# Kernel tuning notes

Hardware: AMD Instinct MI355X
Metric: run time of the kernel (lower is better)

## Reference

```python
import jax, jax.numpy as jnp
import numpy as np

OUT_SIZE = 7      # roi_layer out_size
SAMPLE_NUM = 2    # roi_layer sample_num
STRIDES = (4, 8, 16, 32)
IMG = 1024.0


def _roi_align(feat_nchw, rois, out, scale, sn):
    """mmdet RoIAlign (aligned=False), vectorized over all rois.

    feat_nchw: [B, C, H, W]; rois: [N, 5] = (batch_idx, x1, y1, x2, y2).
    Returns [N, C, out, out].
    """
    feat = jnp.transpose(feat_nchw, (0, 2, 3, 1))  # [B, H, W, C]
    B, H, W, C = feat.shape
    N = rois.shape[0]
    b = rois[:, 0].astype(jnp.int32)
    x1 = rois[:, 1] * scale
    y1 = rois[:, 2] * scale
    x2 = rois[:, 3] * scale
    y2 = rois[:, 4] * scale
    roi_w = jnp.maximum(x2 - x1, 1.0)
    roi_h = jnp.maximum(y2 - y1, 1.0)
    # sample-point offsets within the roi, in bin units: [out*sn]
    grid = (jnp.arange(out, dtype=jnp.float32)[:, None]
            + (jnp.arange(sn, dtype=jnp.float32)[None, :] + 0.5) / sn).reshape(-1)
    ys = y1[:, None] + grid[None, :] * (roi_h / out)[:, None]  # [N, S]
    xs = x1[:, None] + grid[None, :] * (roi_w / out)[:, None]  # [N, S]

    def interp1(coord, size):
        valid = ((coord > -1.0) & (coord < size)).astype(coord.dtype)
        c = jnp.clip(coord, 0.0, size - 1.0)
        lo = jnp.floor(c).astype(jnp.int32)
        hi = jnp.minimum(lo + 1, size - 1)
        w_hi = c - lo.astype(coord.dtype)
        w_lo = 1.0 - w_hi
        # zero-out out-of-image samples via the weights
        return lo, hi, w_lo * valid, w_hi * valid

    y_lo, y_hi, wy_lo, wy_hi = interp1(ys, H)
    x_lo, x_hi, wx_lo, wx_hi = interp1(xs, W)

    def gather(yi, xi):
        # [N, S, S, C]
        return feat[b[:, None, None], yi[:, :, None], xi[:, None, :]]

    val = (gather(y_lo, x_lo) * (wy_lo[:, :, None] * wx_lo[:, None, :])[..., None]
           + gather(y_lo, x_hi) * (wy_lo[:, :, None] * wx_hi[:, None, :])[..., None]
           + gather(y_hi, x_lo) * (wy_hi[:, :, None] * wx_lo[:, None, :])[..., None]
           + gather(y_hi, x_hi) * (wy_hi[:, :, None] * wx_hi[:, None, :])[..., None])
    # average the sn x sn samples inside each bin
    val = val.reshape(N, out, sn, out, sn, C).mean(axis=(2, 4))  # [N, out, out, C]
    return jnp.transpose(val, (0, 3, 1, 2))  # [N, C, out, out]


def setup_inputs() -> dict:
    key = jax.random.key(0)
    ks = jax.random.split(key, 8)
    feats = {}
    for i, hw in enumerate([256, 128, 64, 32]):
        feats[f"feat{i}"] = jax.random.normal(ks[i], (1, 256, hw, hw), dtype=jnp.float32)
    N = 1000
    u = jax.random.uniform(ks[4], (N, 4), dtype=jnp.float32)
    x1 = u[:, 0] * (IMG - 64.0)
    y1 = u[:, 1] * (IMG - 64.0)
    w = 16.0 + u[:, 2] * 480.0
    h = 16.0 + u[:, 3] * 480.0
    x2 = jnp.minimum(x1 + w, IMG - 1.0)
    y2 = jnp.minimum(y1 + h, IMG - 1.0)
    bidx = jnp.zeros((N,), dtype=jnp.float32)
    rois = jnp.stack([bidx, x1, y1, x2, y2], axis=1)
    feats["rois"] = rois
    return feats


def reference(feat0, feat1, feat2, feat3, rois):
    feats = (feat0, feat1, feat2, feat3)
    # PASingleRoIExtractor multi-level path: RoIAlign every roi on every level,
    # then elementwise max across levels.
    out = _roi_align(feats[0], rois, OUT_SIZE, 1.0 / STRIDES[0], SAMPLE_NUM)
    for lvl in range(1, len(feats)):
        out = jnp.maximum(out, _roi_align(feats[lvl], rois, OUT_SIZE,
                                          1.0 / STRIDES[lvl], SAMPLE_NUM))
    return out
```

## Files before the change

kernel.cpp:

```cpp
#include <hip/hip_runtime.h>


#define NCH 256
#define NBIN 49

__device__ __constant__ int   d_H[4]      = {256, 128, 64, 32};
__device__ __constant__ float d_scale[4]  = {0.25f, 0.125f, 0.0625f, 0.03125f};
__device__ __constant__ int   d_off4[4]   = {0, 2097152, 2621440, 2752512};
__device__ __constant__ size_t d_offu[4]  = {0, 16777216, 20971520, 22020096};
__device__ __constant__ int   d_tstart[4] = {0, 4096, 5120, 5376};
__device__ __constant__ int   d_tilesx[4] = {4, 2, 1, 1};

__device__ __forceinline__ unsigned rne_bf16(float v) {
    unsigned b = __float_as_uint(v);
    b += 0x7fffu + ((b >> 16) & 1u);
    return b >> 16;
}

__device__ __forceinline__ int4 make_entry(float coord, int size, int mult) {
    float valid = (coord > -1.0f && coord < (float)size) ? 1.0f : 0.0f;
    float c = fminf(fmaxf(coord, 0.0f), (float)size - 1.0f);
    int lo = (int)floorf(c);
    int hi = min(lo + 1, size - 1);
    float whi = (c - (float)lo) * valid;
    float wlo = (1.0f - (c - (float)lo)) * valid;
    int4 r;
    r.x = lo * mult;
    r.y = hi * mult;
    r.z = __float_as_int(wlo);
    r.w = __float_as_int(whi);
    return r;
}

__device__ __forceinline__ void acc8(float* acc, uint4 u, float w) {
    acc[0] = fmaf(w, __uint_as_float(u.x << 16),         acc[0]);
    acc[1] = fmaf(w, __uint_as_float(u.x & 0xffff0000u), acc[1]);
    acc[2] = fmaf(w, __uint_as_float(u.y << 16),         acc[2]);
    acc[3] = fmaf(w, __uint_as_float(u.y & 0xffff0000u), acc[3]);
    acc[4] = fmaf(w, __uint_as_float(u.z << 16),         acc[4]);
    acc[5] = fmaf(w, __uint_as_float(u.z & 0xffff0000u), acc[5]);
    acc[6] = fmaf(w, __uint_as_float(u.w << 16),         acc[6]);
    acc[7] = fmaf(w, __uint_as_float(u.w & 0xffff0000u), acc[7]);
}

__device__ __forceinline__ void do_sample(const uint4* __restrict__ base,
                                          float* acc, int4 ye, int4 xe) {
    float wyl = __int_as_float(ye.z), wyh = __int_as_float(ye.w);
    float wxl = __int_as_float(xe.z), wxh = __int_as_float(xe.w);
    uint4 ull = base[ye.x + xe.x];
    uint4 ulh = base[ye.x + xe.y];
    uint4 uhl = base[ye.y + xe.x];
    uint4 uhh = base[ye.y + xe.y];
    acc8(acc, ull, wyl * wxl);
    acc8(acc, ulh, wyl * wxh);
    acc8(acc, uhl, wyh * wxl);
    acc8(acc, uhh, wyh * wxh);
}

__global__ __launch_bounds__(256) void transpose_fused(
    const float* __restrict__ f0, const float* __restrict__ f1,
    const float* __restrict__ f2, const float* __restrict__ f3,
    unsigned short* __restrict__ out) {
    __shared__ float tile[64][65];

    const int bid = blockIdx.x;
    const int lvl = (bid >= d_tstart[1]) + (bid >= d_tstart[2]) + (bid >= d_tstart[3]);
    int rem = bid - d_tstart[lvl];
    const int H = d_H[lvl];
    const int tnx = d_tilesx[lvl];
    const int xt = rem % tnx; rem /= tnx;
    const int y  = rem % H;
    const int cg = rem / H;
    const int W = H;
    const int x0 = xt * 64;
    const float* in = (lvl == 0) ? f0 : (lvl == 1) ? f1 : (lvl == 2) ? f2 : f3;
    unsigned short* o = out + d_offu[lvl];

    const int tid = threadIdx.x;
    const int tx = tid & 63;
    const int tq = tid >> 6;
    const size_t HW = (size_t)H * W;
    const float* inp = in + (size_t)(cg * 64) * HW + (size_t)y * W + x0;
    const bool xin = (x0 + tx) < W;
#pragma unroll
    for (int r = 0; r < 16; ++r) {
        int cl = tq * 16 + r;
        tile[cl][tx] = xin ? inp[(size_t)cl * HW + tx] : 0.0f;
    }
    __syncthreads();

    const int o8 = tid & 7;
    const int xi = tid >> 3;
#pragma unroll
    for (int pass = 0; pass < 2; ++pass) {
        int px = xi + pass * 32;
        int x = x0 + px;
        if (x < W) {
            unsigned w0, w1, w2, w3;
            w0 = rne_bf16(tile[o8 * 8 + 0][px]) | (rne_bf16(tile[o8 * 8 + 1][px]) << 16);
            w1 = rne_bf16(tile[o8 * 8 + 2][px]) | (rne_bf16(tile[o8 * 8 + 3][px]) << 16);
            w2 = rne_bf16(tile[o8 * 8 + 4][px]) | (rne_bf16(tile[o8 * 8 + 5][px]) << 16);
            w3 = rne_bf16(tile[o8 * 8 + 6][px]) | (rne_bf16(tile[o8 * 8 + 7][px]) << 16);
            uint4* dst = (uint4*)(o + (size_t)(y * W + x) * NCH + cg * 64 + o8 * 8);
            *dst = make_uint4(w0, w1, w2, w3);
        }
    }
}

__global__ __launch_bounds__(256) void roi_main2(
    const uint4* __restrict__ ws, const float* __restrict__ rois,
    float* __restrict__ out) {
    __shared__ float4 smem4[128 * NBIN / 4];
    __shared__ int4 tbl[4][2][14];
    float* smem = (float*)smem4;

    const int n    = blockIdx.x >> 1;
    const int half = blockIdx.x & 1;
    const int tid  = threadIdx.x;
    const float* r = rois + (size_t)n * 5;

    if (tid < 112) {
        int lvl = tid / 28;
        int e = tid % 28;
        int axis = e / 14;
        int s = e % 14;
        int H = d_H[lvl];
        float sc = d_scale[lvl];
        float a  = (axis ? r[1] : r[2]) * sc;
        float b2 = (axis ? r[3] : r[4]) * sc;
        float binsz = fmaxf(b2 - a, 1.0f) * (1.0f / 7.0f);
        float g = (float)(s >> 1) + 0.25f + 0.5f * (float)(s & 1);
        float coord = a + g * binsz;
        int mult = axis ? 32 : H * 32;
        tbl[lvl][axis][s] = make_entry(coord, H, mult);
    }
    __syncthreads();

    const int p = tid & 15;
    const int h = tid >> 4;
    const int octet = half * 16 + p;
    const int bstart = (h * NBIN) >> 4;
    const int bend   = ((h + 1) * NBIN) >> 4;

    for (int b = bstart; b < bend; ++b) {
        int by = b / 7;
        int bx = b - by * 7;
        float m[8];
#pragma unroll
        for (int k = 0; k < 8; ++k) m[k] = -3.402823e38f;
#pragma unroll
        for (int lvl = 0; lvl < 4; ++lvl) {
            const uint4* base = ws + d_off4[lvl] + octet;
            int4 ye0 = tbl[lvl][0][2 * by];
            int4 ye1 = tbl[lvl][0][2 * by + 1];
            int4 xe0 = tbl[lvl][1][2 * bx];
            int4 xe1 = tbl[lvl][1][2 * bx + 1];
            float acc[8];
#pragma unroll
            for (int k = 0; k < 8; ++k) acc[k] = 0.0f;
            do_sample(base, acc, ye0, xe0);
            do_sample(base, acc, ye0, xe1);
            do_sample(base, acc, ye1, xe0);
            do_sample(base, acc, ye1, xe1);
#pragma unroll
            for (int k = 0; k < 8; ++k) m[k] = fmaxf(m[k], acc[k] * 0.25f);
        }
#pragma unroll
        for (int k = 0; k < 8; ++k) smem[(p * 8 + k) * NBIN + b] = m[k];
    }
    __syncthreads();

    float4* o4 = (float4*)(out + (size_t)n * (NCH * NBIN) + (size_t)half * (128 * NBIN));
    for (int i = tid; i < 128 * NBIN / 4; i += 256) o4[i] = smem4[i];
}

__global__ __launch_bounds__(256) void roi_direct(
    const float* __restrict__ f0, const float* __restrict__ f1,
    const float* __restrict__ f2, const float* __restrict__ f3,
    const float* __restrict__ rois, float* __restrict__ out) {
    const int n = blockIdx.x;
    const int c = threadIdx.x;
    const float* feats[4] = {f0, f1, f2, f3};
    const float* r = rois + (size_t)n * 5;
    for (int b = 0; b < NBIN; ++b) {
        int by = b / 7;
        int bx = b - by * 7;
        float m = -3.402823e38f;
#pragma unroll
        for (int lvl = 0; lvl < 4; ++lvl) {
            int H = d_H[lvl];
            float sc = d_scale[lvl];
            float x1 = r[1] * sc, y1 = r[2] * sc, x2 = r[3] * sc, y2 = r[4] * sc;
            float bw = fmaxf(x2 - x1, 1.0f) * (1.0f / 7.0f);
            float bh = fmaxf(y2 - y1, 1.0f) * (1.0f / 7.0f);
            const float* f = feats[lvl] + (size_t)c * H * H;
            float acc = 0.0f;
#pragma unroll
            for (int sy = 0; sy < 2; ++sy) {
#pragma unroll
                for (int sx = 0; sx < 2; ++sx) {
                    float yc = y1 + ((float)by + 0.25f + 0.5f * sy) * bh;
                    float xc = x1 + ((float)bx + 0.25f + 0.5f * sx) * bw;
                    int4 ey = make_entry(yc, H, H);
                    int4 ex = make_entry(xc, H, 1);
                    float wyl = __int_as_float(ey.z), wyh = __int_as_float(ey.w);
                    float wxl = __int_as_float(ex.z), wxh = __int_as_float(ex.w);
                    acc += f[ey.x + ex.x] * wyl * wxl + f[ey.x + ex.y] * wyl * wxh
                         + f[ey.y + ex.x] * wyh * wxl + f[ey.y + ex.y] * wyh * wxh;
                }
            }
            m = fmaxf(m, acc * 0.25f);
        }
        out[((size_t)n * NCH + c) * NBIN + b] = m;
    }
}

extern "C" void kernel_launch(void* const* d_in, const int* in_sizes, int n_in,
                              void* d_out, int out_size, void* d_ws, size_t ws_size,
                              hipStream_t stream) {
    const float* f0 = (const float*)d_in[0];
    const float* f1 = (const float*)d_in[1];
    const float* f2 = (const float*)d_in[2];
    const float* f3 = (const float*)d_in[3];
    const float* rois = (const float*)d_in[4];
    const int nrois = in_sizes[4] / 5;
    float* out = (float*)d_out;

    const size_t need = 44564480;
    if (ws_size >= need) {
        unsigned short* ws = (unsigned short*)d_ws;
        transpose_fused<<<5504, 256, 0, stream>>>(f0, f1, f2, f3, ws);
        roi_main2<<<2 * nrois, 256, 0, stream>>>((const uint4*)d_ws, rois, out);
    } else {
        roi_direct<<<nrois, 256, 0, stream>>>(f0, f1, f2, f3, rois, out);
    }
}
```

Measured before the change: 247.2 us.

## Switch workspace to fp16 with fdot2 accumulation and split each ROI into quarter-channel blocks

The channel-last workspace now holds fp16 instead of bf16, and the bilinear accumulation uses packed fp16 weights with the fdot2 instruction, so two taps are combined per instruction. The transpose loads use float2 with a padded tile. The ROI kernel now launches four blocks per ROI, each covering 64 channels, which doubles parallelism and shrinks shared memory per block. In exchange the fp16 weights and products carry reduced precision and overflow risk, and the per-ROI table setup is repeated across more blocks.

```diff
diff --git a/kernel.cpp b/kernel.cpp
--- a/kernel.cpp
+++ b/kernel.cpp
@@ -4,20 +4,209 @@
 #define NCH 256
 #define NBIN 49
 
-__device__ __constant__ int   d_H[4]      = {256, 128, 64, 32};
-__device__ __constant__ float d_scale[4]  = {0.25f, 0.125f, 0.0625f, 0.03125f};
-__device__ __constant__ int   d_off4[4]   = {0, 2097152, 2621440, 2752512};
-__device__ __constant__ size_t d_offu[4]  = {0, 16777216, 20971520, 22020096};
-__device__ __constant__ int   d_tstart[4] = {0, 4096, 5120, 5376};
-__device__ __constant__ int   d_tilesx[4] = {4, 2, 1, 1};
-
-__device__ __forceinline__ unsigned rne_bf16(float v) {
-    unsigned b = __float_as_uint(v);
-    b += 0x7fffu + ((b >> 16) & 1u);
-    return b >> 16;
-}
-
-__device__ __forceinline__ int4 make_entry(float coord, int size, int mult) {
+typedef _Float16 half2v __attribute__((ext_vector_type(2)));
+
+#if defined(__has_builtin)
+#if __has_builtin(__builtin_amdgcn_fdot2)
+#define HAVE_FDOT2 1
+#endif
+#if __has_builtin(__builtin_amdgcn_cvt_pkrtz)
+#define HAVE_PKRTZ 1
+#endif
+#endif
+
+__device__ __constant__ int    d_H[4]      = {256, 128, 64, 32};
+__device__ __constant__ float  d_scale[4]  = {0.25f, 0.125f, 0.0625f, 0.03125f};
+__device__ __constant__ int    d_off4[4]   = {0, 2097152, 2621440, 2752512};
+__device__ __constant__ size_t d_offu[4]   = {0, 16777216, 20971520, 22020096};
+__device__ __constant__ int    d_tstart[4] = {0, 4096, 5120, 5376};
+__device__ __constant__ int    d_tilesx[4] = {4, 2, 1, 1};
+
+__device__ __forceinline__ int pack_h2(float a, float b) {
+#ifdef HAVE_PKRTZ
+    return __builtin_bit_cast(int, __builtin_amdgcn_cvt_pkrtz(a, b));
+#else
+    half2v h;
+    h.x = (_Float16)a;
+    h.y = (_Float16)b;
+    return __builtin_bit_cast(int, h);
+#endif
+}
+__device__ __forceinline__ half2v bc_h2(int x) { return __builtin_bit_cast(half2v, x); }
+__device__ __forceinline__ half2v bc_h2u(unsigned x) { return __builtin_bit_cast(half2v, x); }
+
+#ifdef HAVE_FDOT2
+#define ACC2(uLLc, uLHc, w2, k0)                                                                       \
+    acc[k0] = __builtin_amdgcn_fdot2(bc_h2u(__builtin_amdgcn_perm((uLHc), (uLLc), 0x05040100u)), (w2), \
+                                     acc[k0], false);                                                  \
+    acc[k0 + 1] = __builtin_amdgcn_fdot2(                                                              \
+        bc_h2u(__builtin_amdgcn_perm((uLHc), (uLLc), 0x07060302u)), (w2), acc[k0 + 1], false)
+#else
+#define ACC2(uLLc, uLHc, w2, k0)                                       \
+    do {                                                               \
+        half2v a_ = bc_h2u(uLLc), b_ = bc_h2u(uLHc);                   \
+        float w0_ = (float)(w2).x, w1_ = (float)(w2).y;                \
+        acc[k0]     = fmaf((float)a_.x, w0_, acc[k0]);                 \
+        acc[k0]     = fmaf((float)b_.x, w1_, acc[k0]);                 \
+        acc[k0 + 1] = fmaf((float)a_.y, w0_, acc[k0 + 1]);             \
+        acc[k0 + 1] = fmaf((float)b_.y, w1_, acc[k0 + 1]);             \
+    } while (0)
+#endif
+
+__device__ __forceinline__ void do_sample(const uint4* __restrict__ base, float* acc, int4 ye,
+                                          int4 xe) {
+    uint4 uLL = base[ye.x + xe.x];
+    uint4 uLH = base[ye.x + xe.y];
+    uint4 uHL = base[ye.y + xe.x];
+    uint4 uHH = base[ye.y + xe.y];
+    half2v wx = bc_h2(xe.z);
+    half2v wlo = bc_h2(ye.z) * wx;
+    half2v whi = bc_h2(ye.w) * wx;
+    ACC2(uLL.x, uLH.x, wlo, 0);
+    ACC2(uLL.y, uLH.y, wlo, 2);
+    ACC2(uLL.z, uLH.z, wlo, 4);
+    ACC2(uLL.w, uLH.w, wlo, 6);
+    ACC2(uHL.x, uHH.x, whi, 0);
+    ACC2(uHL.y, uHH.y, whi, 2);
+    ACC2(uHL.z, uHH.z, whi, 4);
+    ACC2(uHL.w, uHH.w, whi, 6);
+}
+
+__global__ __launch_bounds__(256) void transpose_fused(
+    const float* __restrict__ f0, const float* __restrict__ f1, const float* __restrict__ f2,
+    const float* __restrict__ f3, unsigned short* __restrict__ out) {
+    __shared__ float tile[64 * 66];
+
+    const int bid = blockIdx.x;
+    const int lvl = (bid >= d_tstart[1]) + (bid >= d_tstart[2]) + (bid >= d_tstart[3]);
+    int rem = bid - d_tstart[lvl];
+    const int H = d_H[lvl];
+    const int tnx = d_tilesx[lvl];
+    const int xt = rem % tnx;
+    rem /= tnx;
+    const int y = rem % H;
+    const int cg = rem / H;
+    const int x0 = xt * 64;
+    const float* in = (lvl == 0) ? f0 : (lvl == 1) ? f1 : (lvl == 2) ? f2 : f3;
+    unsigned short* o = out + d_offu[lvl];
+
+    const int tid = threadIdx.x;
+    const int tx2 = tid & 31;
+    const int wv = tid >> 5;
+    const size_t HW = (size_t)H * H;
+    const float* inp = in + (size_t)(cg * 64) * HW + (size_t)y * H + x0;
+    const bool xin = (x0 + tx2 * 2) < H;
+#pragma unroll
+    for (int r = 0; r < 8; ++r) {
+        int cl = wv * 8 + r;
+        float2 v = make_float2(0.0f, 0.0f);
+        if (xin) v = *(const float2*)(inp + (size_t)cl * HW + tx2 * 2);
+        *(float2*)&tile[cl * 66 + tx2 * 2] = v;
+    }
+    __syncthreads();
+
+    const int o8 = tid & 7;
+    const int xi = tid >> 3;
+#pragma unroll
+    for (int pass = 0; pass < 2; ++pass) {
+        int px = xi + pass * 32;
+        int x = x0 + px;
+        if (x < H) {
+            const float* col = &tile[o8 * 8 * 66 + px];
+            unsigned d0 = (unsigned)pack_h2(col[0 * 66], col[1 * 66]);
+            unsigned d1 = (unsigned)pack_h2(col[2 * 66], col[3 * 66]);
+            unsigned d2 = (unsigned)pack_h2(col[4 * 66], col[5 * 66]);
+            unsigned d3 = (unsigned)pack_h2(col[6 * 66], col[7 * 66]);
+            uint4* dst = (uint4*)(o + (size_t)(y * H + x) * NCH + cg * 64 + o8 * 8);
+            *dst = make_uint4(d0, d1, d2, d3);
+        }
+    }
+}
+
+__global__ __launch_bounds__(256) void roi_main4(const uint4* __restrict__ ws,
+                                                 const float* __restrict__ rois,
+                                                 float* __restrict__ out) {
+    __shared__ float smem[64 * NBIN];
+    __shared__ int4 tbl[4][2][14];
+
+    const int n = blockIdx.x >> 2;
+    const int quarter = blockIdx.x & 3;
+    const int tid = threadIdx.x;
+    const float* r = rois + (size_t)n * 5;
+
+    if (tid < 112) {
+        int lvl = tid / 28;
+        int e = tid % 28;
+        int axis = e / 14;
+        int s = e % 14;
+        int H = d_H[lvl];
+        float sc = d_scale[lvl];
+        float a = (axis ? r[1] : r[2]) * sc;
+        float b2 = (axis ? r[3] : r[4]) * sc;
+        float binsz = fmaxf(b2 - a, 1.0f) * (1.0f / 7.0f);
+        float g = (float)(s >> 1) + 0.25f + 0.5f * (float)(s & 1);
+        float coord = a + g * binsz;
+        float valid = (coord > -1.0f && coord < (float)H) ? 1.0f : 0.0f;
+        float c = fminf(fmaxf(coord, 0.0f), (float)H - 1.0f);
+        int lo = (int)floorf(c);
+        int hi = min(lo + 1, H - 1);
+        float whi = (c - (float)lo) * valid;
+        float wlo = (1.0f - (c - (float)lo)) * valid;
+        int mult = axis ? 32 : H * 32;
+        int4 t;
+        t.x = lo * mult;
+        t.y = hi * mult;
+        if (axis) {
+            t.z = pack_h2(wlo, whi);
+            t.w = 0;
+        } else {
+            t.z = pack_h2(wlo, wlo);
+            t.w = pack_h2(whi, whi);
+        }
+        tbl[lvl][axis][s] = t;
+    }
+    __syncthreads();
+
+    const int p = tid & 7;
+    const int h = tid >> 3;
+    const int octet = quarter * 8 + p;
+    const int bstart = (h * NBIN) >> 5;
+    const int bend = ((h + 1) * NBIN) >> 5;
+
+    for (int b = bstart; b < bend; ++b) {
+        int by = b / 7;
+        int bx = b - by * 7;
+        float m[8];
+#pragma unroll
+        for (int k = 0; k < 8; ++k) m[k] = -3.402823e38f;
+#pragma unroll
+        for (int lvl = 0; lvl < 4; ++lvl) {
+            const uint4* base = ws + d_off4[lvl] + octet;
+            int4 ye0 = tbl[lvl][0][2 * by];
+            int4 ye1 = tbl[lvl][0][2 * by + 1];
+            int4 xe0 = tbl[lvl][1][2 * bx];
+            int4 xe1 = tbl[lvl][1][2 * bx + 1];
+            float acc[8];
+#pragma unroll
+            for (int k = 0; k < 8; ++k) acc[k] = 0.0f;
+            do_sample(base, acc, ye0, xe0);
+            do_sample(base, acc, ye0, xe1);
+            do_sample(base, acc, ye1, xe0);
+            do_sample(base, acc, ye1, xe1);
+#pragma unroll
+            for (int k = 0; k < 8; ++k) m[k] = fmaxf(m[k], acc[k] * 0.25f);
+        }
+#pragma unroll
+        for (int k = 0; k < 8; ++k) smem[(p * 8 + k) * NBIN + b] = m[k];
+    }
+    __syncthreads();
+
+    float4* o4 = (float4*)(out + (size_t)n * (NCH * NBIN) + (size_t)quarter * (64 * NBIN));
+    const float4* s4 = (const float4*)smem;
+    for (int i = tid; i < 64 * NBIN / 4; i += 256) o4[i] = s4[i];
+}
+
+__device__ __forceinline__ int4 make_entry_f(float coord, int size, int mult) {
     float valid = (coord > -1.0f && coord < (float)size) ? 1.0f : 0.0f;
     float c = fminf(fmaxf(coord, 0.0f), (float)size - 1.0f);
     int lo = (int)floorf(c);
@@ -32,152 +221,9 @@
     return r;
 }
 
-__device__ __forceinline__ void acc8(float* acc, uint4 u, float w) {
-    acc[0] = fmaf(w, __uint_as_float(u.x << 16),         acc[0]);
-    acc[1] = fmaf(w, __uint_as_float(u.x & 0xffff0000u), acc[1]);
-    acc[2] = fmaf(w, __uint_as_float(u.y << 16),         acc[2]);
-    acc[3] = fmaf(w, __uint_as_float(u.y & 0xffff0000u), acc[3]);
-    acc[4] = fmaf(w, __uint_as_float(u.z << 16),         acc[4]);
-    acc[5] = fmaf(w, __uint_as_float(u.z & 0xffff0000u), acc[5]);
-    acc[6] = fmaf(w, __uint_as_float(u.w << 16),         acc[6]);
-    acc[7] = fmaf(w, __uint_as_float(u.w & 0xffff0000u), acc[7]);
-}
-
-__device__ __forceinline__ void do_sample(const uint4* __restrict__ base,
-                                          float* acc, int4 ye, int4 xe) {
-    float wyl = __int_as_float(ye.z), wyh = __int_as_float(ye.w);
-    float wxl = __int_as_float(xe.z), wxh = __int_as_float(xe.w);
-    uint4 ull = base[ye.x + xe.x];
-    uint4 ulh = base[ye.x + xe.y];
-    uint4 uhl = base[ye.y + xe.x];
-    uint4 uhh = base[ye.y + xe.y];
-    acc8(acc, ull, wyl * wxl);
-    acc8(acc, ulh, wyl * wxh);
-    acc8(acc, uhl, wyh * wxl);
-    acc8(acc, uhh, wyh * wxh);
-}
-
-__global__ __launch_bounds__(256) void transpose_fused(
-    const float* __restrict__ f0, const float* __restrict__ f1,
-    const float* __restrict__ f2, const float* __restrict__ f3,
-    unsigned short* __restrict__ out) {
-    __shared__ float tile[64][65];
-
-    const int bid = blockIdx.x;
-    const int lvl = (bid >= d_tstart[1]) + (bid >= d_tstart[2]) + (bid >= d_tstart[3]);
-    int rem = bid - d_tstart[lvl];
-    const int H = d_H[lvl];
-    const int tnx = d_tilesx[lvl];
-    const int xt = rem % tnx; rem /= tnx;
-    const int y  = rem % H;
-    const int cg = rem / H;
-    const int W = H;
-    const int x0 = xt * 64;
-    const float* in = (lvl == 0) ? f0 : (lvl == 1) ? f1 : (lvl == 2) ? f2 : f3;
-    unsigned short* o = out + d_offu[lvl];
-
-    const int tid = threadIdx.x;
-    const int tx = tid & 63;
-    const int tq = tid >> 6;
-    const size_t HW = (size_t)H * W;
-    const float* inp = in + (size_t)(cg * 64) * HW + (size_t)y * W + x0;
-    const bool xin = (x0 + tx) < W;
-#pragma unroll
-    for (int r = 0; r < 16; ++r) {
-        int cl = tq * 16 + r;
-        tile[cl][tx] = xin ? inp[(size_t)cl * HW + tx] : 0.0f;
-    }
-    __syncthreads();
-
-    const int o8 = tid & 7;
-    const int xi = tid >> 3;
-#pragma unroll
-    for (int pass = 0; pass < 2; ++pass) {
-        int px = xi + pass * 32;
-        int x = x0 + px;
-        if (x < W) {
-            unsigned w0, w1, w2, w3;
-            w0 = rne_bf16(tile[o8 * 8 + 0][px]) | (rne_bf16(tile[o8 * 8 + 1][px]) << 16);
-            w1 = rne_bf16(tile[o8 * 8 + 2][px]) | (rne_bf16(tile[o8 * 8 + 3][px]) << 16);
-            w2 = rne_bf16(tile[o8 * 8 + 4][px]) | (rne_bf16(tile[o8 * 8 + 5][px]) << 16);
-            w3 = rne_bf16(tile[o8 * 8 + 6][px]) | (rne_bf16(tile[o8 * 8 + 7][px]) << 16);
-            uint4* dst = (uint4*)(o + (size_t)(y * W + x) * NCH + cg * 64 + o8 * 8);
-            *dst = make_uint4(w0, w1, w2, w3);
-        }
-    }
-}
-
-__global__ __launch_bounds__(256) void roi_main2(
-    const uint4* __restrict__ ws, const float* __restrict__ rois,
-    float* __restrict__ out) {
-    __shared__ float4 smem4[128 * NBIN / 4];
-    __shared__ int4 tbl[4][2][14];
-    float* smem = (float*)smem4;
-
-    const int n    = blockIdx.x >> 1;
-    const int half = blockIdx.x & 1;
-    const int tid  = threadIdx.x;
-    const float* r = rois + (size_t)n * 5;
-
-    if (tid < 112) {
-        int lvl = tid / 28;
-        int e = tid % 28;
-        int axis = e / 14;
-        int s = e % 14;
-        int H = d_H[lvl];
-        float sc = d_scale[lvl];
-        float a  = (axis ? r[1] : r[2]) * sc;
-        float b2 = (axis ? r[3] : r[4]) * sc;
-        float binsz = fmaxf(b2 - a, 1.0f) * (1.0f / 7.0f);
-        float g = (float)(s >> 1) + 0.25f + 0.5f * (float)(s & 1);
-        float coord = a + g * binsz;
-        int mult = axis ? 32 : H * 32;
-        tbl[lvl][axis][s] = make_entry(coord, H, mult);
-    }
-    __syncthreads();
-
-    const int p = tid & 15;
-    const int h = tid >> 4;
-    const int octet = half * 16 + p;
-    const int bstart = (h * NBIN) >> 4;
-    const int bend   = ((h + 1) * NBIN) >> 4;
-
-    for (int b = bstart; b < bend; ++b) {
-        int by = b / 7;
-        int bx = b - by * 7;
-        float m[8];
-#pragma unroll
-        for (int k = 0; k < 8; ++k) m[k] = -3.402823e38f;
-#pragma unroll
-        for (int lvl = 0; lvl < 4; ++lvl) {
-            const uint4* base = ws + d_off4[lvl] + octet;
-            int4 ye0 = tbl[lvl][0][2 * by];
-            int4 ye1 = tbl[lvl][0][2 * by + 1];
-            int4 xe0 = tbl[lvl][1][2 * bx];
-            int4 xe1 = tbl[lvl][1][2 * bx + 1];
-            float acc[8];
-#pragma unroll
-            for (int k = 0; k < 8; ++k) acc[k] = 0.0f;
-            do_sample(base, acc, ye0, xe0);
-            do_sample(base, acc, ye0, xe1);
-            do_sample(base, acc, ye1, xe0);
-            do_sample(base, acc, ye1, xe1);
-#pragma unroll
-            for (int k = 0; k < 8; ++k) m[k] = fmaxf(m[k], acc[k] * 0.25f);
-        }
-#pragma unroll
-        for (int k = 0; k < 8; ++k) smem[(p * 8 + k) * NBIN + b] = m[k];
-    }
-    __syncthreads();
-
-    float4* o4 = (float4*)(out + (size_t)n * (NCH * NBIN) + (size_t)half * (128 * NBIN));
-    for (int i = tid; i < 128 * NBIN / 4; i += 256) o4[i] = smem4[i];
-}
-
 __global__ __launch_bounds__(256) void roi_direct(
-    const float* __restrict__ f0, const float* __restrict__ f1,
-    const float* __restrict__ f2, const float* __restrict__ f3,
-    const float* __restrict__ rois, float* __restrict__ out) {
+    const float* __restrict__ f0, const float* __restrict__ f1, const float* __restrict__ f2,
+    const float* __restrict__ f3, const float* __restrict__ rois, float* __restrict__ out) {
     const int n = blockIdx.x;
     const int c = threadIdx.x;
     const float* feats[4] = {f0, f1, f2, f3};
@@ -201,12 +247,12 @@
                 for (int sx = 0; sx < 2; ++sx) {
                     float yc = y1 + ((float)by + 0.25f + 0.5f * sy) * bh;
                     float xc = x1 + ((float)bx + 0.25f + 0.5f * sx) * bw;
-                    int4 ey = make_entry(yc, H, H);
-                    int4 ex = make_entry(xc, H, 1);
+                    int4 ey = make_entry_f(yc, H, H);
+                    int4 ex = make_entry_f(xc, H, 1);
                     float wyl = __int_as_float(ey.z), wyh = __int_as_float(ey.w);
                     float wxl = __int_as_float(ex.z), wxh = __int_as_float(ex.w);
-                    acc += f[ey.x + ex.x] * wyl * wxl + f[ey.x + ex.y] * wyl * wxh
-                         + f[ey.y + ex.x] * wyh * wxl + f[ey.y + ex.y] * wyh * wxh;
+                    acc += f[ey.x + ex.x] * wyl * wxl + f[ey.x + ex.y] * wyl * wxh +
+                           f[ey.y + ex.x] * wyh * wxl + f[ey.y + ex.y] * wyh * wxh;
                 }
             }
             m = fmaxf(m, acc * 0.25f);
@@ -215,9 +261,8 @@
     }
 }
 
-extern "C" void kernel_launch(void* const* d_in, const int* in_sizes, int n_in,
-                              void* d_out, int out_size, void* d_ws, size_t ws_size,
-                              hipStream_t stream) {
+extern "C" void kernel_launch(void* const* d_in, const int* in_sizes, int n_in, void* d_out,
+                              int out_size, void* d_ws, size_t ws_size, hipStream_t stream) {
     const float* f0 = (const float*)d_in[0];
     const float* f1 = (const float*)d_in[1];
     const float* f2 = (const float*)d_in[2];
@@ -230,7 +275,7 @@
     if (ws_size >= need) {
         unsigned short* ws = (unsigned short*)d_ws;
         transpose_fused<<<5504, 256, 0, stream>>>(f0, f1, f2, f3, ws);
-        roi_main2<<<2 * nrois, 256, 0, stream>>>((const uint4*)d_ws, rois, out);
+        roi_main4<<<4 * nrois, 256, 0, stream>>>((const uint4*)d_ws, rois, out);
     } else {
         roi_direct<<<nrois, 256, 0, stream>>>(f0, f1, f2, f3, rois, out);
     }
```

After: 217.0 us. 1.14x faster.
